# Performance work log

Measured on AMD Instinct MI355X. Metric: run time of the kernel, lower is better.

Reference implementation:

```python
import jax, jax.numpy as jnp
import numpy as np
import math

H = 16  # number of heads (init kwarg h)
EPS = 1e-6


def _apply_kernel(x, orf):
    # x: [B, h, L, d_k], orf: [m, d_k]
    m, d_k = orf.shape
    proj = jnp.einsum('bhld,md->bhlm', x, orf) / (d_k ** 0.25)
    norm = jnp.sum(x * x, axis=-1, keepdims=True) / (2.0 * math.sqrt(d_k))
    return (jnp.exp(proj - norm) + EPS) / math.sqrt(m)


def setup_inputs() -> dict:
    key = jax.random.key(0)
    ks = jax.random.split(key, 10)
    B, L, D, m = 4, 4096, 1024, 256
    d_k = D // H
    s = 1.0 / math.sqrt(D)
    return {
        'x': jax.random.normal(ks[0], (B, L, D), jnp.float32),
        'Wq': jax.random.normal(ks[1], (D, D), jnp.float32) * s,
        'bq': jax.random.normal(ks[2], (D,), jnp.float32) * s,
        'Wk': jax.random.normal(ks[3], (D, D), jnp.float32) * s,
        'bk': jax.random.normal(ks[4], (D,), jnp.float32) * s,
        'Wv': jax.random.normal(ks[5], (D, D), jnp.float32) * s,
        'bv': jax.random.normal(ks[6], (D,), jnp.float32) * s,
        'Wo': jax.random.normal(ks[7], (D, D), jnp.float32) * s,
        'bo': jax.random.normal(ks[8], (D,), jnp.float32) * s,
        'orf': jax.random.normal(ks[9], (m, d_k), jnp.float32),
    }


def reference(x, Wq, bq, Wk, bk, Wv, bv, Wo, bo, orf):
    B, L, D = x.shape
    d_k = D // H

    def split(y):  # [B, L, D] -> [B, h, L, d_k]
        return y.reshape(B, L, H, d_k).transpose(0, 2, 1, 3)

    q = split(x @ Wq.T + bq)
    k = split(x @ Wk.T + bk)
    v = split(x @ Wv.T + bv)

    q_phi = _apply_kernel(q, orf)  # [B, h, L, m]
    k_phi = _apply_kernel(k, orf)  # [B, h, L, m]

    # FAVOR+ linear attention: O(L*m*d_k)
    kv = jnp.einsum('bhlm,bhld->bhmd', k_phi, v)      # [B, h, m, d_k]
    ksum = jnp.sum(k_phi, axis=2)                      # [B, h, m]
    num = jnp.einsum('bhlm,bhmd->bhld', q_phi, kv)     # [B, h, L, d_k]
    den = jnp.einsum('bhlm,bhm->bhl', q_phi, ksum)     # [B, h, L]
    out = num / den[..., None]

    out = out.transpose(0, 2, 1, 3).reshape(B, L, D)   # concat heads
    return out @ Wo.T + bo
```

## Files before the change

kernel.cpp:

```cpp
#include <hip/hip_runtime.h>
#include <math.h>

#define HH 16
#define BB 4
#define LL 4096
#define DD 1024
#define DK 64
#define MMF 256
#define EPSF 1e-6f
#define KSCALE (0.35355339059327373f * 1.4426950408889634f)
#define NORMSCALE (0.0625f * 1.4426950408889634f)
#define NSPLIT 8
#define LCH (LL / NSPLIT)

typedef __attribute__((ext_vector_type(8))) short bf16x8;
typedef __attribute__((ext_vector_type(4))) float f32x4;
typedef __attribute__((ext_vector_type(8))) unsigned short u16x8;

__device__ __forceinline__ unsigned short f2bf(float f) {
  union { float f; unsigned u; } v; v.f = f;
  unsigned r = v.u + 0x7FFF + ((v.u >> 16) & 1);
  return (unsigned short)(r >> 16);
}
__device__ __forceinline__ float bf2f(unsigned short h) {
  union { unsigned u; float f; } v; v.u = ((unsigned)h) << 16;
  return v.f;
}
__device__ __forceinline__ f32x4 mfma16(bf16x8 a, bf16x8 b, f32x4 c) {
  return __builtin_amdgcn_mfma_f32_16x16x32_bf16(a, b, c, 0, 0, 0);
}
__device__ __forceinline__ void gload16(const unsigned short* g, unsigned short* l) {
  __builtin_amdgcn_global_load_lds(
      (const __attribute__((address_space(1))) void*)g,
      (__attribute__((address_space(3))) void*)l, 16, 0, 0);
}
#define SWZ(row, col) ((col) ^ (((row) & 7) << 3))

__global__ __launch_bounds__(256) void cvt_bf16(
    const float* __restrict__ src, unsigned short* __restrict__ dst, int n) {
  int i = (blockIdx.x * 256 + threadIdx.x) * 4;
  if (i < n) {
    float4 v = *(const float4*)&src[i];
    ushort4 o;
    o.x = f2bf(v.x); o.y = f2bf(v.y); o.z = f2bf(v.z); o.w = f2bf(v.w);
    *(ushort4*)&dst[i] = o;
  }
}

__global__ __launch_bounds__(256) void cvt_bf16_w(
    const float* __restrict__ W0, const float* __restrict__ W1,
    const float* __restrict__ W2, const float* __restrict__ W3,
    unsigned short* __restrict__ D0, unsigned short* __restrict__ D1,
    unsigned short* __restrict__ D2, unsigned short* __restrict__ D3) {
  const float* s;
  unsigned short* d;
  switch (blockIdx.y) {
    case 0: s = W0; d = D0; break;
    case 1: s = W1; d = D1; break;
    case 2: s = W2; d = D2; break;
    default: s = W3; d = D3; break;
  }
  int i = (blockIdx.x * 256 + threadIdx.x) * 4;
  float4 v = *(const float4*)&s[i];
  ushort4 o;
  o.x = f2bf(v.x); o.y = f2bf(v.y); o.z = f2bf(v.z); o.w = f2bf(v.w);
  *(ushort4*)&d[i] = o;
}

__global__ __launch_bounds__(256) void cvt_orf(
    const float* __restrict__ src, unsigned short* __restrict__ hi,
    unsigned short* __restrict__ lo, int n) {
  int i = blockIdx.x * 256 + threadIdx.x;
  if (i < n) {
    float f = src[i] * KSCALE;
    unsigned short h = f2bf(f);
    hi[i] = h;
    lo[i] = f2bf(f - bf2f(h));
  }
}

template <int MODE>
__global__ __launch_bounds__(256) void gemm_mfma(
    const unsigned short* __restrict__ A, const unsigned short* __restrict__ W,
    const float* __restrict__ bias, float* __restrict__ Cf,
    unsigned short* __restrict__ C1, unsigned short* __restrict__ C2,
    float* __restrict__ Cn, int M, int N, int K) {
  __shared__ __align__(16) char smem[65536];
  unsigned short* S = (unsigned short*)smem;
  const int tid = threadIdx.x, lane = tid & 63;
  const int w = tid >> 6, wr = w >> 1, wc = w & 1;
  const int g = lane >> 4, li = lane & 15;
  const int flat = blockIdx.y * gridDim.x + blockIdx.x;
  const int xcd = flat & 7, loc = flat >> 3;
  const int m0 = ((xcd << 4) + (loc & 15)) * 128;
  const int n0 = (loc >> 4) * 128;

  f32x4 acc[4][4] = {};
  const int srow8 = lane >> 3;
  const int scol  = ((lane & 7) ^ srow8) << 3;
  const unsigned short* Ag = A + (size_t)(m0 + w * 32 + srow8) * K + scol;
  const unsigned short* Wg = W + (size_t)(n0 + w * 32 + srow8) * K + scol;
  const int nt = K >> 6;

#pragma unroll
  for (int j = 0; j < 4; ++j) {
    gload16(Ag + (size_t)j * 8 * K, S + (w * 32 + j * 8) * 64);
    gload16(Wg + (size_t)j * 8 * K, S + 8192 + (w * 32 + j * 8) * 64);
  }

  for (int t = 0; t < nt; ++t) {
    const int co = (t & 1) << 14;
    const int no = co ^ 16384;
    if (t + 1 < nt) {
      const int k1 = (t + 1) << 6;
#pragma unroll
      for (int j = 0; j < 4; ++j) {
        gload16(Ag + (size_t)j * 8 * K + k1, S + no + (w * 32 + j * 8) * 64);
        gload16(Wg + (size_t)j * 8 * K + k1, S + no + 8192 + (w * 32 + j * 8) * 64);
      }
      asm volatile("s_waitcnt vmcnt(8)" ::: "memory");
    } else {
      asm volatile("s_waitcnt vmcnt(0)" ::: "memory");
    }
    __builtin_amdgcn_s_barrier();

    const int sx = (li & 7) << 3;
#pragma unroll
    for (int kk = 0; kk < 2; ++kk) {
      const int c = (kk * 32 + g * 8) ^ sx;
      bf16x8 af[4], bfr[4];
#pragma unroll
      for (int i = 0; i < 4; ++i)
        af[i] = *(const bf16x8*)&S[co + (wr * 64 + i * 16 + li) * 64 + c];
#pragma unroll
      for (int j = 0; j < 4; ++j)
        bfr[j] = *(const bf16x8*)&S[co + 8192 + (wc * 64 + j * 16 + li) * 64 + c];
#pragma unroll
      for (int i = 0; i < 4; ++i)
#pragma unroll
        for (int j = 0; j < 4; ++j)
          acc[i][j] = mfma16(af[i], bfr[j], acc[i][j]);
    }
    asm volatile("s_waitcnt lgkmcnt(0)" ::: "memory");
    __builtin_amdgcn_s_barrier();
  }

  float* ep = (float*)smem + w * (32 * 68);
  const int head = (n0 + wc * 64) >> 6;
  const int rbase = m0 + wr * 64;
  const int b = rbase >> 12;

  if (MODE == 2) {
#pragma unroll
    for (int jh = 0; jh < 2; ++jh) {
#pragma unroll
      for (int i2 = 0; i2 < 2; ++i2) {
        const int i = jh * 2 + i2;
#pragma unroll
        for (int j = 0; j < 4; ++j) {
          const float bz = bias[n0 + wc * 64 + j * 16 + li];
#pragma unroll
          for (int r = 0; r < 4; ++r)
            ep[(i2 * 16 + 4 * g + r) * 68 + j * 16 + li] = acc[i][j][r] + bz;
        }
      }
      const int rrow = lane >> 3, cc = lane & 7;
#pragma unroll
      for (int p = 0; p < 4; ++p) {
        const int row = p * 8 + rrow;
        float v[8];
        *(f32x4*)&v[0] = *(const f32x4*)&ep[row * 68 + cc * 8];
        *(f32x4*)&v[4] = *(const f32x4*)&ep[row * 68 + cc * 8 + 4];
        float np = 0.f;
        u16x8 hv, lv;
#pragma unroll
        for (int e = 0; e < 8; ++e) {
          float vv = v[e];
          np += vv * vv;
          unsigned short h = f2bf(vv);
          hv[e] = h;
          lv[e] = f2bf(vv - bf2f(h));
        }
        const int lg = (rbase + jh * 32 + row) & 4095;
        const size_t rowb = (size_t)(b * 16 + head) * 4096 + lg;
        *(u16x8*)&C1[rowb * 64 + cc * 8] = hv;
        *(u16x8*)&C2[rowb * 64 + cc * 8] = lv;
        np += __shfl_xor(np, 1);
        np += __shfl_xor(np, 2);
        np += __shfl_xor(np, 4);
        if (cc == 0) Cn[rowb] = np * NORMSCALE;
      }
    }
  } else if (MODE == 1) {
#pragma unroll
    for (int jh = 0; jh < 2; ++jh) {
#pragma unroll
      for (int i = 0; i < 4; ++i)
#pragma unroll
        for (int j2 = 0; j2 < 2; ++j2) {
          const int j = jh * 2 + j2;
          const float bz = bias[n0 + wc * 64 + j * 16 + li];
          f32x4 t;
          t[0] = acc[i][j][0] + bz; t[1] = acc[i][j][1] + bz;
          t[2] = acc[i][j][2] + bz; t[3] = acc[i][j][3] + bz;
          *(f32x4*)&ep[(j2 * 16 + li) * 68 + i * 16 + 4 * g] = t;
        }
      const int rd = lane >> 3, cc = lane & 7;
#pragma unroll
      for (int p = 0; p < 4; ++p) {
        const int dl = p * 8 + rd;
        float v[8];
        *(f32x4*)&v[0] = *(const f32x4*)&ep[dl * 68 + cc * 8];
        *(f32x4*)&v[4] = *(const f32x4*)&ep[dl * 68 + cc * 8 + 4];
        u16x8 hv;
#pragma unroll
        for (int e = 0; e < 8; ++e) hv[e] = f2bf(v[e]);
        const int dh = jh * 32 + dl;
        const int lg = rbase & 4095;
        *(u16x8*)&C1[((size_t)(b * 16 + head) * 64 + dh) * 4096 + lg + cc * 8] = hv;
      }
    }
  } else {
#pragma unroll
    for (int jh = 0; jh < 2; ++jh) {
#pragma unroll
      for (int i2 = 0; i2 < 2; ++i2) {
        const int i = jh * 2 + i2;
#pragma unroll
        for (int j = 0; j < 4; ++j) {
          const float bz = bias[n0 + wc * 64 + j * 16 + li];
#pragma unroll
          for (int r = 0; r < 4; ++r)
            ep[(i2 * 16 + 4 * g + r) * 68 + j * 16 + li] = acc[i][j][r] + bz;
        }
      }
      const int rrow = lane >> 4, cc = lane & 15;
#pragma unroll
      for (int p = 0; p < 8; ++p) {
        const int row = p * 4 + rrow;
        f32x4 v = *(const f32x4*)&ep[row * 68 + cc * 4];
        *(f32x4*)&Cf[(size_t)(rbase + jh * 32 + row) * 1024 + n0 + wc * 64 + cc * 4] = v;
      }
    }
  }
}

__global__ __launch_bounds__(256, 2) void kv_mfma(
    const unsigned short* __restrict__ khi, const unsigned short* __restrict__ klo,
    const float* __restrict__ knorms, const unsigned short* __restrict__ vt,
    const unsigned short* __restrict__ orfhi, const unsigned short* __restrict__ orflo,
    float* __restrict__ pkv, float* __restrict__ pksum) {
  __shared__ __align__(16) unsigned short KsHi[64 * 64], KsLo[64 * 64];
  __shared__ __align__(16) unsigned short VT[64 * 64], KphiT[64 * 64];
  __shared__ float ns[64];
  const int tid = threadIdx.x, lane = tid & 63, w = tid >> 6;
  const int g = lane >> 4, li = lane & 15;
  const int bh = blockIdx.x, sp = blockIdx.y;
  const int srow8 = lane >> 3;
  const int scol  = ((lane & 7) ^ srow8) << 3;
  const int sx = (li & 7) << 3;

  bf16x8 oh[4][2], ol[4][2];
#pragma unroll
  for (int p = 0; p < 4; ++p)
#pragma unroll
    for (int kk = 0; kk < 2; ++kk) {
      const size_t o = (size_t)(p * 64 + w * 16 + li) * 64 + kk * 32 + g * 8;
      oh[p][kk] = *(const bf16x8*)&orfhi[o];
      ol[p][kk] = *(const bf16x8*)&orflo[o];
    }

  f32x4 kvacc[4][4] = {};
  float ksacc[4][4] = {};

  for (int c = 0; c < LCH / 64; ++c) {
    const int l0 = sp * LCH + c * 64;
    __syncthreads();
    {
      const size_t kb = ((size_t)bh * 4096 + l0 + w * 16 + srow8) * 64 + scol;
      gload16(khi + kb, &KsHi[(w * 16) * 64]);
      gload16(khi + kb + 8 * 64, &KsHi[(w * 16 + 8) * 64]);
      gload16(klo + kb, &KsLo[(w * 16) * 64]);
      gload16(klo + kb + 8 * 64, &KsLo[(w * 16 + 8) * 64]);
      const size_t vb = ((size_t)bh * 64 + w * 16 + srow8) * 4096 + l0 + scol;
      gload16(vt + vb, &VT[(w * 16) * 64]);
      gload16(vt + vb + (size_t)8 * 4096, &VT[(w * 16 + 8) * 64]);
      if (tid < 64) ns[tid] = knorms[(size_t)bh * 4096 + l0 + tid];
    }
    __syncthreads();

#pragma unroll
    for (int p = 0; p < 4; ++p) {
      f32x4 pr[4] = {};
      __builtin_amdgcn_s_setprio(1);
#pragma unroll
      for (int kk = 0; kk < 2; ++kk) {
        const int cx = (kk * 32 + g * 8) ^ sx;
#pragma unroll
        for (int lf = 0; lf < 4; ++lf) {
          const bf16x8 bh2 = *(const bf16x8*)&KsHi[(lf * 16 + li) * 64 + cx];
          const bf16x8 bl2 = *(const bf16x8*)&KsLo[(lf * 16 + li) * 64 + cx];
          pr[lf] = mfma16(oh[p][kk], bh2, pr[lf]);
          pr[lf] = mfma16(oh[p][kk], bl2, pr[lf]);
          pr[lf] = mfma16(ol[p][kk], bh2, pr[lf]);
        }
      }
      __builtin_amdgcn_s_setprio(0);
#pragma unroll
      for (int lf = 0; lf < 4; ++lf) {
        const float nrm = ns[lf * 16 + li];
#pragma unroll
        for (int r = 0; r < 4; ++r) {
          float phi = exp2f(pr[lf][r] - nrm) + EPSF;
          ksacc[p][r] += phi;
          const int row = w * 16 + 4 * g + r;
          KphiT[row * 64 + SWZ(row, lf * 16 + li)] = f2bf(phi);
        }
      }
      __builtin_amdgcn_s_setprio(1);
#pragma unroll
      for (int kk = 0; kk < 2; ++kk) {
        const int cx = (kk * 32 + g * 8) ^ sx;
        const bf16x8 a = *(const bf16x8*)&KphiT[(w * 16 + li) * 64 + cx];
#pragma unroll
        for (int df = 0; df < 4; ++df) {
          const bf16x8 bv = *(const bf16x8*)&VT[(df * 16 + li) * 64 + cx];
          kvacc[p][df] = mfma16(a, bv, kvacc[p][df]);
        }
      }
      __builtin_amdgcn_s_setprio(0);
    }
  }
  float* kvo = pkv + ((size_t)sp * 64 + bh) * (MMF * DK);
#pragma unroll
  for (int p = 0; p < 4; ++p)
#pragma unroll
    for (int df = 0; df < 4; ++df)
#pragma unroll
      for (int r = 0; r < 4; ++r)
        kvo[(p * 64 + w * 16 + 4 * g + r) * DK + df * 16 + li] = kvacc[p][df][r];

  float* kso = pksum + ((size_t)sp * 64 + bh) * MMF;
#pragma unroll
  for (int p = 0; p < 4; ++p)
#pragma unroll
    for (int r = 0; r < 4; ++r) {
      float s = ksacc[p][r];
      s += __shfl_xor(s, 1); s += __shfl_xor(s, 2);
      s += __shfl_xor(s, 4); s += __shfl_xor(s, 8);
      if (li == 0) kso[p * 64 + w * 16 + 4 * g + r] = s;
    }
}

__global__ __launch_bounds__(256) void reduce_parts(
    const float* __restrict__ pkv, unsigned short* __restrict__ kvT,
    const float* __restrict__ pks, float* __restrict__ ksg) {
  const int id = blockIdx.x * 256 + threadIdx.x;
  {
    const int bh = id >> 12, rest = id & 4095;
    const int m0 = (rest >> 6) << 2, d = rest & 63;
    float s0 = 0.f, s1 = 0.f, s2 = 0.f, s3 = 0.f;
#pragma unroll
    for (int sp = 0; sp < NSPLIT; ++sp) {
      const float* p = pkv + (size_t)(sp * 64 + bh) * (MMF * DK) + d;
      s0 += p[(m0 + 0) * DK]; s1 += p[(m0 + 1) * DK];
      s2 += p[(m0 + 2) * DK]; s3 += p[(m0 + 3) * DK];
    }
    ushort4 o;
    o.x = f2bf(s0); o.y = f2bf(s1); o.z = f2bf(s2); o.w = f2bf(s3);
    *(ushort4*)&kvT[((size_t)bh * DK + d) * MMF + m0] = o;
  }
  if (id < 4096) {
    float4 s = {0.f, 0.f, 0.f, 0.f};
#pragma unroll
    for (int sp = 0; sp < NSPLIT; ++sp) {
      float4 v = *(const float4*)&pks[(size_t)sp * 64 * MMF + id * 4];
      s.x += v.x; s.y += v.y; s.z += v.z; s.w += v.w;
    }
    *(float4*)&ksg[id * 4] = s;
  }
}

__global__ __launch_bounds__(512, 4) void qattn_mfma(
    const unsigned short* __restrict__ qhi, const unsigned short* __restrict__ qlo,
    const float* __restrict__ qnorms,
    const unsigned short* __restrict__ orfhi,
    const unsigned short* __restrict__ kvT, const float* __restrict__ ksg,
    unsigned short* __restrict__ attn) {
  __shared__ __align__(16) unsigned short OHi[256 * 64];
  __shared__ __align__(16) unsigned short KvTs[64 * 256];
  __shared__ __align__(16) unsigned short Qphi[8][16 * 64];
  const int tid = threadIdx.x, lane = tid & 63, w = tid >> 6;
  const int g = lane >> 4, li = lane & 15;
  const int bh = blockIdx.x, lb = blockIdx.y;
  const int b = bh >> 4, h = bh & 15;
  const int srow8 = lane >> 3;
  const int scol  = ((lane & 7) ^ srow8) << 3;
  const int sx = (li & 7) << 3;

#pragma unroll
  for (int q = 0; q < 4; ++q) {
    const size_t o = (size_t)(w * 32 + q * 8 + srow8) * 64 + scol;
    gload16(orfhi + o, &OHi[(w * 32 + q * 8) * 64]);
  }
  {
    const int srow2 = lane >> 5;
#pragma unroll
    for (int q = 0; q < 4; ++q) {
      const int d0 = w * 8 + q * 2, dr = d0 + srow2;
      gload16(kvT + ((size_t)bh * DK + dr) * MMF + (((lane & 31) ^ (dr & 7)) << 3),
              &KvTs[d0 * 256]);
    }
  }

  float ksr[4][4];
#pragma unroll
  for (int p = 0; p < 4; ++p)
#pragma unroll
    for (int mf = 0; mf < 4; ++mf)
      ksr[p][mf] = ksg[(size_t)bh * MMF + p * 64 + mf * 16 + li];
  const float4 nr =
      *(const float4*)&qnorms[(size_t)bh * 4096 + lb * 128 + w * 16 + 4 * g];
  bf16x8 qh[2], ql[2];
  {
    const size_t qr = ((size_t)bh * 4096 + lb * 128 + w * 16 + li) * 64 + g * 8;
    qh[0] = *(const bf16x8*)&qhi[qr];
    qh[1] = *(const bf16x8*)&qhi[qr + 32];
    ql[0] = *(const bf16x8*)&qlo[qr];
    ql[1] = *(const bf16x8*)&qlo[qr + 32];
  }
  __syncthreads();

  f32x4 numacc[4] = {};
  float denacc[4] = {};

#pragma unroll
  for (int p = 0; p < 4; ++p) {
    f32x4 pr[4] = {};
    __builtin_amdgcn_s_setprio(1);
#pragma unroll
    for (int kk = 0; kk < 2; ++kk) {
      const int cx = (kk * 32 + g * 8) ^ sx;
#pragma unroll
      for (int mf = 0; mf < 4; ++mf) {
        const int row = p * 64 + mf * 16 + li;
        const bf16x8 bh2 = *(const bf16x8*)&OHi[row * 64 + cx];
        pr[mf] = mfma16(qh[kk], bh2, pr[mf]);
        pr[mf] = mfma16(ql[kk], bh2, pr[mf]);
      }
    }
    __builtin_amdgcn_s_setprio(0);
#pragma unroll
    for (int mf = 0; mf < 4; ++mf) {
      const float ks = ksr[p][mf];
#pragma unroll
      for (int r = 0; r < 4; ++r) {
        float phi = exp2f(pr[mf][r] - nr[r]) + EPSF;
        denacc[r] += phi * ks;
        const int row = 4 * g + r;
        Qphi[w][row * 64 + SWZ(row, mf * 16 + li)] = f2bf(phi);
      }
    }
    __builtin_amdgcn_s_setprio(1);
#pragma unroll
    for (int kk = 0; kk < 2; ++kk) {
      const int cx = (kk * 32 + g * 8) ^ sx;
      const bf16x8 a = *(const bf16x8*)&Qphi[w][li * 64 + cx];
#pragma unroll
      for (int df = 0; df < 4; ++df) {
        const bf16x8 bv = *(const bf16x8*)
            &KvTs[(df * 16 + li) * 256 + (((p * 8 + kk * 4 + g) ^ (li & 7)) << 3)];
        numacc[df] = mfma16(a, bv, numacc[df]);
      }
    }
    __builtin_amdgcn_s_setprio(0);
  }
  float den[4];
#pragma unroll
  for (int r = 0; r < 4; ++r) {
    float s = denacc[r];
    s += __shfl_xor(s, 1); s += __shfl_xor(s, 2);
    s += __shfl_xor(s, 4); s += __shfl_xor(s, 8);
    den[r] = s;
  }
  unsigned short* ab =
      attn + ((size_t)b * 4096 + lb * 128) * 1024 + h * 64;
#pragma unroll
  for (int df = 0; df < 4; ++df)
#pragma unroll
    for (int r = 0; r < 4; ++r)
      ab[(size_t)(w * 16 + 4 * g + r) * 1024 + df * 16 + li] =
          f2bf(numacc[df][r] / den[r]);
}

extern "C" void kernel_launch(void* const* d_in, const int* in_sizes, int n_in,
                              void* d_out, int out_size, void* d_ws, size_t ws_size,
                              hipStream_t stream) {
  (void)in_sizes; (void)n_in; (void)out_size; (void)ws_size;
  const float* x   = (const float*)d_in[0];
  const float* Wq  = (const float*)d_in[1];
  const float* bq  = (const float*)d_in[2];
  const float* Wk  = (const float*)d_in[3];
  const float* bk  = (const float*)d_in[4];
  const float* Wv  = (const float*)d_in[5];
  const float* bv  = (const float*)d_in[6];
  const float* Wo  = (const float*)d_in[7];
  const float* bo  = (const float*)d_in[8];
  const float* orf = (const float*)d_in[9];
  float* out = (float*)d_out;

  const size_t ND = (size_t)BB * LL * DD;
  char* base = (char*)d_ws;
  size_t off = 0;
  auto alloc = [&](size_t bytes) -> char* {
    char* p = base + off;
    off += (bytes + 255) & ~(size_t)255;
    return p;
  };
  unsigned short* wqbf   = (unsigned short*)alloc((size_t)DD * DD * 2);
  unsigned short* wkbf   = (unsigned short*)alloc((size_t)DD * DD * 2);
  unsigned short* wvbf   = (unsigned short*)alloc((size_t)DD * DD * 2);
  unsigned short* wobf   = (unsigned short*)alloc((size_t)DD * DD * 2);
  unsigned short* orfhi  = (unsigned short*)alloc((size_t)MMF * DK * 2);
  unsigned short* orflo  = (unsigned short*)alloc((size_t)MMF * DK * 2);
  unsigned short* xbf    = (unsigned short*)alloc(ND * 2);
  unsigned short* qhi    = (unsigned short*)alloc(ND * 2);
  unsigned short* qlo    = (unsigned short*)alloc(ND * 2);
  unsigned short* khi    = (unsigned short*)alloc(ND * 2);
  unsigned short* klo    = (unsigned short*)alloc(ND * 2);
  unsigned short* vtbuf  = (unsigned short*)alloc(ND * 2);
  float*          qnorms = (float*)alloc((size_t)64 * LL * 4);
  float*          knorms = (float*)alloc((size_t)64 * LL * 4);
  float*          pksum  = (float*)alloc((size_t)NSPLIT * 64 * MMF * 4);
  unsigned short* kvT    = (unsigned short*)alloc((size_t)64 * DK * MMF * 2);
  float*          ksg    = (float*)alloc((size_t)64 * MMF * 4);
  float*          pkv    = (float*)xbf;
  unsigned short* attnbf = khi;

  cvt_bf16<<<16384, 256, 0, stream>>>(x, xbf, (int)ND);
  cvt_bf16_w<<<dim3(1024, 4), 256, 0, stream>>>(Wq, Wk, Wv, Wo,
                                                wqbf, wkbf, wvbf, wobf);
  cvt_orf<<<64, 256, 0, stream>>>(orf, orfhi, orflo, MMF * DK);

  dim3 gg(128, 8);
  gemm_mfma<2><<<gg, 256, 0, stream>>>(xbf, wqbf, bq, (float*)0, qhi, qlo,
                                       qnorms, BB * LL, DD, DD);
  gemm_mfma<2><<<gg, 256, 0, stream>>>(xbf, wkbf, bk, (float*)0, khi, klo,
                                       knorms, BB * LL, DD, DD);
  gemm_mfma<1><<<gg, 256, 0, stream>>>(xbf, wvbf, bv, (float*)0, vtbuf,
                                       (unsigned short*)0, (float*)0,
                                       BB * LL, DD, DD);

  kv_mfma<<<dim3(64, NSPLIT), 256, 0, stream>>>(khi, klo, knorms, vtbuf,
                                                orfhi, orflo, pkv, pksum);
  reduce_parts<<<1024, 256, 0, stream>>>(pkv, kvT, pksum, ksg);
  qattn_mfma<<<dim3(64, 32), 512, 0, stream>>>(qhi, qlo, qnorms, orfhi,
                                               kvT, ksg, attnbf);

  gemm_mfma<0><<<gg, 256, 0, stream>>>(attnbf, wobf, bo, out, (unsigned short*)0,
                                       (unsigned short*)0, (float*)0,
                                       BB * LL, DD, DD);
}
```

Baseline: 312.9 us.

## Double-buffer K/V tiles in kv_mfma and preload all key norms

Splits the K hi/lo and V-transposed shared-memory tiles into two buffers so the next chunk's global-to-LDS loads are issued before computing on the current chunk, with explicit vmcnt/lgkmcnt waits and raw barriers in place of __syncthreads. All 512 key norms for the split are loaded into shared memory once up front instead of per chunk. This hides global load latency behind MFMA work, at the cost of more LDS per block, which could lower occupancy. It also relies on hand-placed waitcnt counts being correct.

Result: no change. 313.5 us (+0.2%).

```diff
diff --git a/kernel.cpp b/kernel.cpp
--- a/kernel.cpp
+++ b/kernel.cpp
@@ -250,9 +250,10 @@
     const float* __restrict__ knorms, const unsigned short* __restrict__ vt,
     const unsigned short* __restrict__ orfhi, const unsigned short* __restrict__ orflo,
     float* __restrict__ pkv, float* __restrict__ pksum) {
-  __shared__ __align__(16) unsigned short KsHi[64 * 64], KsLo[64 * 64];
-  __shared__ __align__(16) unsigned short VT[64 * 64], KphiT[64 * 64];
-  __shared__ float ns[64];
+  __shared__ __align__(16) unsigned short KsHi[2][64 * 64], KsLo[2][64 * 64];
+  __shared__ __align__(16) unsigned short VT[2][64 * 64];
+  __shared__ __align__(16) unsigned short KphiT[64 * 64];
+  __shared__ float ns[512];
   const int tid = threadIdx.x, lane = tid & 63, w = tid >> 6;
   const int g = lane >> 4, li = lane & 15;
   const int bh = blockIdx.x, sp = blockIdx.y;
@@ -270,24 +271,40 @@
       ol[p][kk] = *(const bf16x8*)&orflo[o];
     }
 
+  ns[tid]       = knorms[(size_t)bh * 4096 + sp * LCH + tid];
+  ns[tid + 256] = knorms[(size_t)bh * 4096 + sp * LCH + 256 + tid];
+
+  const size_t kbase = ((size_t)bh * 4096 + sp * LCH + w * 16 + srow8) * 64 + scol;
+  const size_t vbase = ((size_t)bh * 64 + w * 16 + srow8) * 4096 + sp * LCH + scol;
+
+  gload16(khi + kbase, &KsHi[0][(w * 16) * 64]);
+  gload16(khi + kbase + 8 * 64, &KsHi[0][(w * 16 + 8) * 64]);
+  gload16(klo + kbase, &KsLo[0][(w * 16) * 64]);
+  gload16(klo + kbase + 8 * 64, &KsLo[0][(w * 16 + 8) * 64]);
+  gload16(vt + vbase, &VT[0][(w * 16) * 64]);
+  gload16(vt + vbase + (size_t)8 * 4096, &VT[0][(w * 16 + 8) * 64]);
+  asm volatile("s_waitcnt lgkmcnt(0)" ::: "memory");
+
   f32x4 kvacc[4][4] = {};
   float ksacc[4][4] = {};
 
   for (int c = 0; c < LCH / 64; ++c) {
-    const int l0 = sp * LCH + c * 64;
-    __syncthreads();
-    {
-      const size_t kb = ((size_t)bh * 4096 + l0 + w * 16 + srow8) * 64 + scol;
-      gload16(khi + kb, &KsHi[(w * 16) * 64]);
-      gload16(khi + kb + 8 * 64, &KsHi[(w * 16 + 8) * 64]);
-      gload16(klo + kb, &KsLo[(w * 16) * 64]);
-      gload16(klo + kb + 8 * 64, &KsLo[(w * 16 + 8) * 64]);
-      const size_t vb = ((size_t)bh * 64 + w * 16 + srow8) * 4096 + l0 + scol;
-      gload16(vt + vb, &VT[(w * 16) * 64]);
-      gload16(vt + vb + (size_t)8 * 4096, &VT[(w * 16 + 8) * 64]);
-      if (tid < 64) ns[tid] = knorms[(size_t)bh * 4096 + l0 + tid];
-    }
-    __syncthreads();
+    const int cur = c & 1;
+    if (c + 1 < LCH / 64) {
+      const int nb = cur ^ 1;
+      const size_t ko = kbase + (size_t)(c + 1) * 64 * 64;
+      const size_t vo = vbase + (size_t)(c + 1) * 64;
+      gload16(khi + ko, &KsHi[nb][(w * 16) * 64]);
+      gload16(khi + ko + 8 * 64, &KsHi[nb][(w * 16 + 8) * 64]);
+      gload16(klo + ko, &KsLo[nb][(w * 16) * 64]);
+      gload16(klo + ko + 8 * 64, &KsLo[nb][(w * 16 + 8) * 64]);
+      gload16(vt + vo, &VT[nb][(w * 16) * 64]);
+      gload16(vt + vo + (size_t)8 * 4096, &VT[nb][(w * 16 + 8) * 64]);
+      asm volatile("s_waitcnt vmcnt(6)" ::: "memory");
+    } else {
+      asm volatile("s_waitcnt vmcnt(0)" ::: "memory");
+    }
+    __builtin_amdgcn_s_barrier();
 
 #pragma unroll
     for (int p = 0; p < 4; ++p) {
@@ -298,8 +315,8 @@
         const int cx = (kk * 32 + g * 8) ^ sx;
 #pragma unroll
         for (int lf = 0; lf < 4; ++lf) {
-          const bf16x8 bh2 = *(const bf16x8*)&KsHi[(lf * 16 + li) * 64 + cx];
-          const bf16x8 bl2 = *(const bf16x8*)&KsLo[(lf * 16 + li) * 64 + cx];
+          const bf16x8 bh2 = *(const bf16x8*)&KsHi[cur][(lf * 16 + li) * 64 + cx];
+          const bf16x8 bl2 = *(const bf16x8*)&KsLo[cur][(lf * 16 + li) * 64 + cx];
           pr[lf] = mfma16(oh[p][kk], bh2, pr[lf]);
           pr[lf] = mfma16(oh[p][kk], bl2, pr[lf]);
           pr[lf] = mfma16(ol[p][kk], bh2, pr[lf]);
@@ -308,7 +325,7 @@
       __builtin_amdgcn_s_setprio(0);
 #pragma unroll
       for (int lf = 0; lf < 4; ++lf) {
-        const float nrm = ns[lf * 16 + li];
+        const float nrm = ns[c * 64 + lf * 16 + li];
 #pragma unroll
         for (int r = 0; r < 4; ++r) {
           float phi = exp2f(pr[lf][r] - nrm) + EPSF;
@@ -324,12 +341,14 @@
         const bf16x8 a = *(const bf16x8*)&KphiT[(w * 16 + li) * 64 + cx];
 #pragma unroll
         for (int df = 0; df < 4; ++df) {
-          const bf16x8 bv = *(const bf16x8*)&VT[(df * 16 + li) * 64 + cx];
+          const bf16x8 bv = *(const bf16x8*)&VT[cur][(df * 16 + li) * 64 + cx];
           kvacc[p][df] = mfma16(a, bv, kvacc[p][df]);
         }
       }
       __builtin_amdgcn_s_setprio(0);
     }
+    asm volatile("s_waitcnt lgkmcnt(0)" ::: "memory");
+    __builtin_amdgcn_s_barrier();
   }
   float* kvo = pkv + ((size_t)sp * 64 + bh) * (MMF * DK);
 #pragma unroll
```
